# Kernel tuning notes

Measured on AMD Instinct MI355X. Metric: run time of the kernel, lower is better.

The kernel has to match this reference:

```python
import jax, jax.numpy as jnp
import numpy as np

NUM_HEADS = 8


def _nearest_idx(x, x_grid):
    # x: [b,n,dx]; x_grid: [b,H,W,dx] regular grid -> flat nearest cell index [b,n]
    b = x.shape[0]
    H, W = x_grid.shape[1], x_grid.shape[2]
    gf = x_grid.reshape(b, H * W, -1)
    lo = gf[:, :1]   # min corner [b,1,dx]
    hi = gf[:, -1:]  # max corner [b,1,dx]
    dims = jnp.asarray([H, W], dtype=x.dtype)
    t = (x - lo) / (hi - lo) * (dims - 1.0)
    idx = jnp.clip(jnp.round(t), 0.0, dims - 1.0).astype(jnp.int32)  # [b,n,2]
    return idx[..., 0] * W + idx[..., 1]


def _cumcount(idx):
    # per-batch cumulative count of each value, in order of appearance
    b, n = idx.shape
    order = jnp.argsort(idx, axis=1, stable=True)
    s = jnp.take_along_axis(idx, order, axis=1)
    ar = jnp.arange(n)
    new_run = jnp.concatenate([jnp.ones((b, 1), bool), s[:, 1:] != s[:, :-1]], axis=1)
    run_start = jax.lax.cummax(jnp.where(new_run, ar, 0), axis=1)
    cc_sorted = (ar - run_start).astype(jnp.int32)
    return jnp.zeros((b, n), jnp.int32).at[jnp.arange(b)[:, None], order].set(cc_sorted)


def _mhca(q_in, kv, mask, Wq, Wk, Wv, Wo):
    # q_in: [B,1,e]; kv: [B,K,e]; mask: [B,K] (True = attend)
    B, K, e = kv.shape
    dh = e // NUM_HEADS
    q = (q_in @ Wq).reshape(B, 1, NUM_HEADS, dh)
    k = (kv @ Wk).reshape(B, K, NUM_HEADS, dh)
    v = (kv @ Wv).reshape(B, K, NUM_HEADS, dh)
    scores = jnp.einsum('bqhd,bkhd->bhqk', q, k) / jnp.sqrt(jnp.asarray(dh, q.dtype))
    scores = jnp.where(mask[:, None, None, :], scores, jnp.finfo(scores.dtype).min)
    attn = jax.nn.softmax(scores, axis=-1)
    out = jnp.einsum('bhqk,bkhd->bqhd', attn, v).reshape(B, 1, e)
    return out @ Wo


def setup_inputs() -> dict:
    key = jax.random.key(0)
    ks = jax.random.split(key, 8)
    b, n, e, H, W = 8, 8192, 128, 64, 64
    x = jax.random.uniform(ks[0], (b, n, 2), jnp.float32)
    z = jax.random.normal(ks[1], (b, n, e), jnp.float32)
    g0 = jnp.linspace(0.0, 1.0, H)
    g1 = jnp.linspace(0.0, 1.0, W)
    mg = jnp.stack(jnp.meshgrid(g0, g1, indexing='ij'), axis=-1)  # [H,W,2]
    x_grid = jnp.broadcast_to(mg, (b, H, W, 2)).astype(jnp.float32)
    z_grid = jax.random.normal(ks[2], (b, H, W, e), jnp.float32)
    latent = jax.random.normal(ks[3], (e,), jnp.float32)
    scale = 1.0 / np.sqrt(e).astype(np.float32)
    Wq = jax.random.normal(ks[4], (e, e), jnp.float32) * scale
    Wk = jax.random.normal(ks[5], (e, e), jnp.float32) * scale
    Wv = jax.random.normal(ks[6], (e, e), jnp.float32) * scale
    Wo = jax.random.normal(ks[7], (e, e), jnp.float32) * scale
    return {"x": x, "z": z, "x_grid": x_grid, "z_grid": z_grid, "latent": latent,
            "Wq": Wq, "Wk": Wk, "Wv": Wv, "Wo": Wo, "max_patch": 20}


def reference(x, z, x_grid, z_grid, latent, Wq, Wk, Wv, Wo, max_patch):
    b, n, e = z.shape
    H, W = x_grid.shape[1], x_grid.shape[2]
    S = H * W
    nearest = _nearest_idx(x, x_grid)                    # [b,n]
    cc = _cumcount(nearest)                              # [b,n]
    bidx = jnp.broadcast_to(jnp.arange(b)[:, None], (b, n))
    valid = cc < max_patch
    slot = jnp.where(valid, cc, 0)
    # ragged scatter: pack each point's z into its grid cell's padded sequence
    joint = jnp.zeros((b, S, max_patch, e), z.dtype)
    joint = joint.at[bidx, nearest, slot].add(z * valid[..., None].astype(z.dtype))
    zg_flat = z_grid.reshape(b, S, e)
    joint = jnp.concatenate([joint, zg_flat[:, :, None, :]], axis=2)  # [b,S,P+1,e]
    counts = jnp.zeros((b, S), jnp.int32).at[bidx, nearest].add(1)
    mask = jnp.arange(max_patch + 1)[None, None, :] < jnp.minimum(counts, max_patch)[..., None]
    mask = mask.at[..., -1].set(True)  # grid token always attended
    joint = joint.reshape(b * S, max_patch + 1, e)
    mask = mask.reshape(b * S, max_patch + 1)
    q = jnp.broadcast_to(latent, (b * S, 1, e))          # z0_grid queries
    zg = _mhca(q, joint, mask, Wq, Wk, Wv, Wo)           # [b*S,1,e]
    zg = zg.reshape(b, H, W, e)
    return x_grid, zg
```

## Files before the change

### kernel.cpp

```cpp
#include <hip/hip_runtime.h>
#include <cstdint>
#include <cstddef>

#define S_CELLS 4096
#define NB      8
#define NPTS    8192
#define E       128
#define MAXP    20
#define NHEADS  8
#define NPT_ROWS 65536
#define NGR_ROWS 32768

#define WS_COUNTS 0
#define WS_SLOTS  131072
#define WS_WT1    2752512
#define WS_WT2    2793472
#define WS_SC     2828288
#define WS_V      5974016

typedef __attribute__((ext_vector_type(8))) short bf16x8;
typedef __attribute__((ext_vector_type(4))) float f32x4;

__device__ __forceinline__ unsigned short f2bf_bits(float f) {
    unsigned u = __float_as_uint(f);
    unsigned rounded = u + 0x7FFFu + ((u >> 16) & 1u);
    return (unsigned short)(rounded >> 16);
}
__device__ __forceinline__ float bf2f(unsigned short u) {
    return __uint_as_float(((unsigned)u) << 16);
}

__global__ void __launch_bounds__(256)
k_prep(const float* __restrict__ x,
       const float* __restrict__ x_grid,
       const float* __restrict__ latent,
       const float* __restrict__ Wq,
       const float* __restrict__ Wk,
       const float* __restrict__ Wv,
       const float* __restrict__ Wo,
       int* __restrict__ counts,
       int* __restrict__ slots,
       unsigned short* __restrict__ WT1,
       unsigned short* __restrict__ WT2,
       float* __restrict__ out_xgrid) {
    const int t   = threadIdx.x;
    const int blk = blockIdx.x;

    if (blk < 256) {
        int i = blk * 256 + t;
        out_xgrid[i] = x_grid[i];
        int b = i >> 13;
        float x0 = x[(size_t)i * 2 + 0];
        float x1 = x[(size_t)i * 2 + 1];
        int i0 = (int)rintf(x0 * 63.0f);
        int i1 = (int)rintf(x1 * 63.0f);
        i0 = min(max(i0, 0), 63);
        i1 = min(max(i1, 0), 63);
        int cell = b * S_CELLS + i0 * 64 + i1;
        int slot = atomicAdd(&counts[cell], 1);
        if (slot < MAXP) slots[(size_t)cell * MAXP + slot] = i & (NPTS - 1);
        return;
    }

    if (blk == 256) {
        __shared__ float lat[E];
        __shared__ float qv[E];
        const int j = t & 127;
        if (t < E) lat[t] = latent[t];
        __syncthreads();
        float acc = 0.0f;
        for (int k2 = 0; k2 < E; ++k2) acc += lat[k2] * Wq[k2 * E + j];
        qv[j] = acc;
        __syncthreads();
        const int hb = (t >> 7) * 4;
        for (int h = hb; h < hb + 4; ++h) {
            float a = 0.0f;
            #pragma unroll
            for (int d = 0; d < 16; ++d) a += Wk[j * E + h * 16 + d] * qv[h * 16 + d];
            WT1[(size_t)(128 + h) * 136 + j] = f2bf_bits(a * 0.25f);
        }
        for (int idx = t; idx < 8 * 136; idx += 256) {
            int rr = idx / 136, cc = idx - rr * 136;
            WT1[(size_t)(136 + rr) * 136 + cc] = 0;
        }
        return;
    }

    {
        const float* W = (blk < 261) ? Wv : Wo;
        unsigned short* WT = (blk < 261) ? WT1 : WT2;
        const int n0 = ((blk - 257) & 3) * 32;
        __shared__ float lbuf[128][33];
        #pragma unroll
        for (int it = 0; it < 16; ++it) {
            int k  = (t >> 5) + it * 8;
            int nl = t & 31;
            lbuf[k][nl] = W[(size_t)k * E + n0 + nl];
        }
        __syncthreads();
        for (int idx = t; idx < 32 * 136; idx += 256) {
            int nl = idx / 136, k = idx - nl * 136;
            float v = (k < 128) ? lbuf[k][nl] : 0.0f;
            WT[(size_t)(n0 + nl) * 136 + k] = f2bf_bits(v);
        }
    }
}

__device__ __forceinline__ bf16x8 load_afrag_f32(const float* __restrict__ X,
                                                 int row, int kq, int q) {
    const float4* xr = (const float4*)(X + (size_t)row * E);
    float4 lo = xr[kq * 8 + q * 2];
    float4 hi = xr[kq * 8 + q * 2 + 1];
    bf16x8 f;
    f[0] = (short)f2bf_bits(lo.x);
    f[1] = (short)f2bf_bits(lo.y);
    f[2] = (short)f2bf_bits(lo.z);
    f[3] = (short)f2bf_bits(lo.w);
    f[4] = (short)f2bf_bits(hi.x);
    f[5] = (short)f2bf_bits(hi.y);
    f[6] = (short)f2bf_bits(hi.z);
    f[7] = (short)f2bf_bits(hi.w);
    return f;
}

__global__ void __launch_bounds__(256)
k_gemm1(const float* __restrict__ Xz,
        const float* __restrict__ Xg,
        const unsigned short* __restrict__ WT1g,
        unsigned short* __restrict__ V,
        float* __restrict__ SC) {
    __shared__ unsigned short W_t[20480];

    const int t = threadIdx.x;
    {
        const float4* src = (const float4*)WT1g;
        float4* dst = (float4*)W_t;
        #pragma unroll
        for (int it = 0; it < 10; ++it) dst[t + it * 256] = src[t + it * 256];
    }
    __syncthreads();

    const int lane = t & 63;
    const int wv   = t >> 6;
    const int cn   = lane & 15;
    const int q    = lane >> 4;

    const int grow0 = blockIdx.x * 128;
    const float* Xsrc;
    int srow;
    if (blockIdx.x < 512) { Xsrc = Xz; srow = grow0; }
    else                  { Xsrc = Xg; srow = grow0 - NPT_ROWS; }

    f32x4 acc[2][9];
    #pragma unroll
    for (int mt = 0; mt < 2; ++mt)
        #pragma unroll
        for (int nt = 0; nt < 9; ++nt)
            acc[mt][nt] = f32x4{0.0f, 0.0f, 0.0f, 0.0f};

    #pragma unroll
    for (int kq = 0; kq < 4; ++kq) {
        bf16x8 a[2];
        #pragma unroll
        for (int mt = 0; mt < 2; ++mt)
            a[mt] = load_afrag_f32(Xsrc, srow + wv * 32 + mt * 16 + cn, kq, q);
        #pragma unroll
        for (int nt = 0; nt < 9; ++nt) {
            const bf16x8 b = *(const bf16x8*)&W_t[(size_t)(nt * 16 + cn) * 136 + kq * 32 + q * 8];
            #pragma unroll
            for (int mt = 0; mt < 2; ++mt)
                acc[mt][nt] = __builtin_amdgcn_mfma_f32_16x16x32_bf16(
                    a[mt], b, acc[mt][nt], 0, 0, 0);
        }
    }

    #pragma unroll
    for (int mt = 0; mt < 2; ++mt) {
        const int rb = grow0 + wv * 32 + mt * 16 + q * 4;
        #pragma unroll
        for (int nt = 0; nt < 8; ++nt)
            #pragma unroll
            for (int r = 0; r < 4; ++r)
                V[(size_t)(rb + r) * E + nt * 16 + cn] = f2bf_bits(acc[mt][nt][r]);
        if (cn < 8) {
            #pragma unroll
            for (int r = 0; r < 4; ++r)
                SC[(size_t)(rb + r) * NHEADS + cn] = acc[mt][8][r];
        }
    }
}

__global__ void __launch_bounds__(256)
k_attn_proj(const int* __restrict__ counts,
            const int* __restrict__ slots,
            const float* __restrict__ SC,
            const unsigned short* __restrict__ Vg,
            const unsigned short* __restrict__ WT2g,
            float* __restrict__ zg) {
    __shared__ unsigned short W_t[17408];
    __shared__ unsigned short X_s[16][136];

    const int t = threadIdx.x;
    {
        const float4* src = (const float4*)WT2g;
        float4* dst = (float4*)W_t;
        #pragma unroll
        for (int it = 0; it < 8; ++it) dst[t + it * 256] = src[t + it * 256];
        if (t < 128) dst[t + 2048] = src[t + 2048];
    }

    const int lane = t & 63;
    const int wv   = t >> 6;
    const int cb   = blockIdx.x * 16;
    const int cw   = cb + wv * 4;
    const int b    = blockIdx.x >> 8;
    const int base = b * NPTS;
    const int h    = lane >> 3;

    int cnt_l = (lane < 16) ? counts[cb + lane] : 0;

    int m4[4], sl[4];
    #pragma unroll
    for (int ci = 0; ci < 4; ++ci) {
        m4[ci] = min(__shfl(cnt_l, wv * 4 + ci, 64), MAXP);
        sl[ci] = (lane < MAXP) ? slots[(size_t)(cw + ci) * MAXP + lane] : 0;
    }

    float mm[4], ss[4], o0[4], o1[4];
    #pragma unroll
    for (int ci = 0; ci < 4; ++ci) {
        size_t r0 = (size_t)(NPT_ROWS + cw + ci);
        mm[ci] = SC[r0 * NHEADS + h];
        unsigned v0 = *(const unsigned*)(Vg + r0 * E + 2 * lane);
        o0[ci] = bf2f((unsigned short)v0);
        o1[ci] = bf2f((unsigned short)(v0 >> 16));
        ss[ci] = 1.0f;
    }

    #pragma unroll
    for (int ci = 0; ci < 4; ++ci) {
        const int m = m4[ci];
        for (int t0 = 0; t0 < m; t0 += 4) {
            float av[4], p0[4], p1[4];
            #pragma unroll
            for (int j = 0; j < 4; ++j) {
                int pt = __shfl(sl[ci], t0 + j, 64);
                bool val = (t0 + j) < m;
                pt = val ? pt : 0;
                size_t r = (size_t)(base + pt);
                float sa = SC[r * NHEADS + h];
                av[j] = val ? sa : -1e30f;
                unsigned vv = *(const unsigned*)(Vg + r * E + 2 * lane);
                p0[j] = bf2f((unsigned short)vv);
                p1[j] = bf2f((unsigned short)(vv >> 16));
            }
            #pragma unroll
            for (int j = 0; j < 4; ++j) {
                float nm = fmaxf(mm[ci], av[j]);
                float e  = __expf(av[j] - nm);
                float al = __expf(mm[ci] - nm);
                ss[ci] = ss[ci] * al + e;
                o0[ci] = o0[ci] * al + e * p0[j];
                o1[ci] = o1[ci] * al + e * p1[j];
                mm[ci] = nm;
            }
        }
        float inv = 1.0f / ss[ci];
        unsigned packed = (unsigned)f2bf_bits(o0[ci] * inv)
                        | ((unsigned)f2bf_bits(o1[ci] * inv) << 16);
        *(unsigned*)&X_s[wv * 4 + ci][2 * lane] = packed;
    }
    __syncthreads();

    const int cn  = lane & 15;
    const int q   = lane >> 4;
    const int nt0 = wv * 2;
    f32x4 acc[2];
    acc[0] = f32x4{0.0f, 0.0f, 0.0f, 0.0f};
    acc[1] = f32x4{0.0f, 0.0f, 0.0f, 0.0f};

    #pragma unroll
    for (int kq = 0; kq < 4; ++kq) {
        bf16x8 a = *(const bf16x8*)&X_s[cn][kq * 32 + q * 8];
        #pragma unroll
        for (int j = 0; j < 2; ++j) {
            const bf16x8 bb = *(const bf16x8*)&W_t[(size_t)((nt0 + j) * 16 + cn) * 136 + kq * 32 + q * 8];
            acc[j] = __builtin_amdgcn_mfma_f32_16x16x32_bf16(a, bb, acc[j], 0, 0, 0);
        }
    }

    const int rb = blockIdx.x * 16 + q * 4;
    #pragma unroll
    for (int j = 0; j < 2; ++j)
        #pragma unroll
        for (int r = 0; r < 4; ++r)
            zg[(size_t)(rb + r) * E + (nt0 + j) * 16 + cn] = acc[j][r];
}

extern "C" void kernel_launch(void* const* d_in, const int* in_sizes, int n_in,
                              void* d_out, int out_size, void* d_ws, size_t ws_size,
                              hipStream_t stream) {
    const float* x      = (const float*)d_in[0];
    const float* z      = (const float*)d_in[1];
    const float* x_grid = (const float*)d_in[2];
    const float* z_grid = (const float*)d_in[3];
    const float* latent = (const float*)d_in[4];
    const float* Wq     = (const float*)d_in[5];
    const float* Wk     = (const float*)d_in[6];
    const float* Wv     = (const float*)d_in[7];
    const float* Wo     = (const float*)d_in[8];

    char* ws = (char*)d_ws;
    int*            counts = (int*)(ws + WS_COUNTS);
    int*            slots  = (int*)(ws + WS_SLOTS);
    unsigned short* WT1    = (unsigned short*)(ws + WS_WT1);
    unsigned short* WT2    = (unsigned short*)(ws + WS_WT2);
    float*          SC     = (float*)(ws + WS_SC);
    unsigned short* V      = (unsigned short*)(ws + WS_V);

    float* out_xgrid = (float*)d_out;
    float* zg        = (float*)d_out + NB * NPTS;

    (void)hipMemsetAsync(counts, 0, NB * S_CELLS * sizeof(int), stream);

    k_prep<<<265, 256, 0, stream>>>(x, x_grid, latent, Wq, Wk, Wv, Wo,
                                    counts, slots, WT1, WT2, out_xgrid);

    k_gemm1<<<768, 256, 0, stream>>>(z, z_grid, WT1, V, SC);

    k_attn_proj<<<2048, 256, 0, stream>>>(counts, slots, SC, V, WT2, zg);
}
```

Measured before the change: 139.9 us.

## Fuse binning into GEMM kernel, drop memset, one wave per cell in attention

Zeroing of the cell counts moves into the small prep kernel, which replaces the memset. The point-binning blocks move into the main GEMM launch so they run alongside the projection work. The attention kernel now uses 1024-thread blocks with one wave per cell, and keeps the Wo fragments in registers loaded straight from global memory instead of staging them in LDS. BF16 packing switches to cheaper round-half-away conversion. This cuts launches, LDS staging and serial per-wave cell loops, at the cost of slightly different rounding and larger blocks that may reduce occupancy flexibility.

```diff
diff --git a/kernel.cpp b/kernel.cpp
--- a/kernel.cpp
+++ b/kernel.cpp
@@ -26,43 +26,37 @@
     unsigned rounded = u + 0x7FFFu + ((u >> 16) & 1u);
     return (unsigned short)(rounded >> 16);
 }
+__device__ __forceinline__ unsigned short f2bf_rta(float f) {
+    return (unsigned short)((__float_as_uint(f) + 0x8000u) >> 16);
+}
+__device__ __forceinline__ unsigned pack_bf2(float a, float b) {
+    unsigned ua = __float_as_uint(a) + 0x8000u;
+    unsigned ub = __float_as_uint(b) + 0x8000u;
+    return (ua >> 16) | (ub & 0xFFFF0000u);
+}
 __device__ __forceinline__ float bf2f(unsigned short u) {
     return __uint_as_float(((unsigned)u) << 16);
 }
 
 __global__ void __launch_bounds__(256)
-k_prep(const float* __restrict__ x,
-       const float* __restrict__ x_grid,
-       const float* __restrict__ latent,
+k_prep(const float* __restrict__ latent,
        const float* __restrict__ Wq,
        const float* __restrict__ Wk,
        const float* __restrict__ Wv,
        const float* __restrict__ Wo,
        int* __restrict__ counts,
-       int* __restrict__ slots,
        unsigned short* __restrict__ WT1,
-       unsigned short* __restrict__ WT2,
-       float* __restrict__ out_xgrid) {
+       unsigned short* __restrict__ WT2) {
     const int t   = threadIdx.x;
     const int blk = blockIdx.x;
 
-    if (blk < 256) {
-        int i = blk * 256 + t;
-        out_xgrid[i] = x_grid[i];
-        int b = i >> 13;
-        float x0 = x[(size_t)i * 2 + 0];
-        float x1 = x[(size_t)i * 2 + 1];
-        int i0 = (int)rintf(x0 * 63.0f);
-        int i1 = (int)rintf(x1 * 63.0f);
-        i0 = min(max(i0, 0), 63);
-        i1 = min(max(i1, 0), 63);
-        int cell = b * S_CELLS + i0 * 64 + i1;
-        int slot = atomicAdd(&counts[cell], 1);
-        if (slot < MAXP) slots[(size_t)cell * MAXP + slot] = i & (NPTS - 1);
-        return;
-    }
-
-    if (blk == 256) {
+    {
+        int4* c4 = (int4*)counts;
+        for (int idx = blk * 256 + t; idx < 8192; idx += 9 * 256)
+            c4[idx] = int4{0, 0, 0, 0};
+    }
+
+    if (blk == 0) {
         __shared__ float lat[E];
         __shared__ float qv[E];
         const int j = t & 127;
@@ -86,23 +80,21 @@
         return;
     }
 
-    {
-        const float* W = (blk < 261) ? Wv : Wo;
-        unsigned short* WT = (blk < 261) ? WT1 : WT2;
-        const int n0 = ((blk - 257) & 3) * 32;
-        __shared__ float lbuf[128][33];
-        #pragma unroll
-        for (int it = 0; it < 16; ++it) {
-            int k  = (t >> 5) + it * 8;
-            int nl = t & 31;
-            lbuf[k][nl] = W[(size_t)k * E + n0 + nl];
-        }
-        __syncthreads();
-        for (int idx = t; idx < 32 * 136; idx += 256) {
-            int nl = idx / 136, k = idx - nl * 136;
-            float v = (k < 128) ? lbuf[k][nl] : 0.0f;
-            WT[(size_t)(n0 + nl) * 136 + k] = f2bf_bits(v);
-        }
+    const float* W = (blk < 5) ? Wv : Wo;
+    unsigned short* WT = (blk < 5) ? WT1 : WT2;
+    const int n0 = ((blk - 1) & 3) * 32;
+    __shared__ float lbuf[128][33];
+    #pragma unroll
+    for (int it = 0; it < 16; ++it) {
+        int k  = (t >> 5) + it * 8;
+        int nl = t & 31;
+        lbuf[k][nl] = W[(size_t)k * E + n0 + nl];
+    }
+    __syncthreads();
+    for (int idx = t; idx < 32 * 136; idx += 256) {
+        int nl = idx / 136, k = idx - nl * 136;
+        float v = (k < 128) ? lbuf[k][nl] : 0.0f;
+        WT[(size_t)(n0 + nl) * 136 + k] = f2bf_bits(v);
     }
 }
 
@@ -111,27 +103,47 @@
     const float4* xr = (const float4*)(X + (size_t)row * E);
     float4 lo = xr[kq * 8 + q * 2];
     float4 hi = xr[kq * 8 + q * 2 + 1];
-    bf16x8 f;
-    f[0] = (short)f2bf_bits(lo.x);
-    f[1] = (short)f2bf_bits(lo.y);
-    f[2] = (short)f2bf_bits(lo.z);
-    f[3] = (short)f2bf_bits(lo.w);
-    f[4] = (short)f2bf_bits(hi.x);
-    f[5] = (short)f2bf_bits(hi.y);
-    f[6] = (short)f2bf_bits(hi.z);
-    f[7] = (short)f2bf_bits(hi.w);
-    return f;
+    unsigned u[4];
+    u[0] = pack_bf2(lo.x, lo.y);
+    u[1] = pack_bf2(lo.z, lo.w);
+    u[2] = pack_bf2(hi.x, hi.y);
+    u[3] = pack_bf2(hi.z, hi.w);
+    union { unsigned u4[4]; bf16x8 v; } cv;
+    cv.u4[0] = u[0]; cv.u4[1] = u[1]; cv.u4[2] = u[2]; cv.u4[3] = u[3];
+    return cv.v;
 }
 
 __global__ void __launch_bounds__(256)
-k_gemm1(const float* __restrict__ Xz,
-        const float* __restrict__ Xg,
-        const unsigned short* __restrict__ WT1g,
-        unsigned short* __restrict__ V,
-        float* __restrict__ SC) {
+k_main(const float* __restrict__ x,
+       const float* __restrict__ x_grid,
+       const float* __restrict__ Xz,
+       const float* __restrict__ Xg,
+       const unsigned short* __restrict__ WT1g,
+       int* __restrict__ counts,
+       int* __restrict__ slots,
+       unsigned short* __restrict__ V,
+       float* __restrict__ SC,
+       float* __restrict__ out_xgrid) {
     __shared__ unsigned short W_t[20480];
 
     const int t = threadIdx.x;
+
+    if (blockIdx.x >= 768) {
+        int i = (blockIdx.x - 768) * 256 + t;
+        out_xgrid[i] = x_grid[i];
+        int b = i >> 13;
+        float x0 = x[(size_t)i * 2 + 0];
+        float x1 = x[(size_t)i * 2 + 1];
+        int i0 = (int)rintf(x0 * 63.0f);
+        int i1 = (int)rintf(x1 * 63.0f);
+        i0 = min(max(i0, 0), 63);
+        i1 = min(max(i1, 0), 63);
+        int cell = b * S_CELLS + i0 * 64 + i1;
+        int slot = atomicAdd(&counts[cell], 1);
+        if (slot < MAXP) slots[(size_t)cell * MAXP + slot] = i & (NPTS - 1);
+        return;
+    }
+
     {
         const float4* src = (const float4*)WT1g;
         float4* dst = (float4*)W_t;
@@ -181,7 +193,7 @@
         for (int nt = 0; nt < 8; ++nt)
             #pragma unroll
             for (int r = 0; r < 4; ++r)
-                V[(size_t)(rb + r) * E + nt * 16 + cn] = f2bf_bits(acc[mt][nt][r]);
+                V[(size_t)(rb + r) * E + nt * 16 + cn] = f2bf_rta(acc[mt][nt][r]);
         if (cn < 8) {
             #pragma unroll
             for (int r = 0; r < 4; ++r)
@@ -190,111 +202,83 @@
     }
 }
 
-__global__ void __launch_bounds__(256)
+__global__ void __launch_bounds__(1024)
 k_attn_proj(const int* __restrict__ counts,
             const int* __restrict__ slots,
             const float* __restrict__ SC,
             const unsigned short* __restrict__ Vg,
             const unsigned short* __restrict__ WT2g,
             float* __restrict__ zg) {
-    __shared__ unsigned short W_t[17408];
-    __shared__ unsigned short X_s[16][136];
-
-    const int t = threadIdx.x;
-    {
-        const float4* src = (const float4*)WT2g;
-        float4* dst = (float4*)W_t;
-        #pragma unroll
-        for (int it = 0; it < 8; ++it) dst[t + it * 256] = src[t + it * 256];
-        if (t < 128) dst[t + 2048] = src[t + 2048];
-    }
-
+    __shared__ __align__(16) unsigned short X_s[16][136];
+
+    const int t    = threadIdx.x;
     const int lane = t & 63;
     const int wv   = t >> 6;
     const int cb   = blockIdx.x * 16;
-    const int cw   = cb + wv * 4;
-    const int b    = blockIdx.x >> 8;
+    const int b    = cb >> 12;
     const int base = b * NPTS;
-    const int h    = lane >> 3;
-
-    int cnt_l = (lane < 16) ? counts[cb + lane] : 0;
-
-    int m4[4], sl[4];
-    #pragma unroll
-    for (int ci = 0; ci < 4; ++ci) {
-        m4[ci] = min(__shfl(cnt_l, wv * 4 + ci, 64), MAXP);
-        sl[ci] = (lane < MAXP) ? slots[(size_t)(cw + ci) * MAXP + lane] : 0;
-    }
-
-    float mm[4], ss[4], o0[4], o1[4];
-    #pragma unroll
-    for (int ci = 0; ci < 4; ++ci) {
-        size_t r0 = (size_t)(NPT_ROWS + cw + ci);
-        mm[ci] = SC[r0 * NHEADS + h];
-        unsigned v0 = *(const unsigned*)(Vg + r0 * E + 2 * lane);
-        o0[ci] = bf2f((unsigned short)v0);
-        o1[ci] = bf2f((unsigned short)(v0 >> 16));
-        ss[ci] = 1.0f;
-    }
-
-    #pragma unroll
-    for (int ci = 0; ci < 4; ++ci) {
-        const int m = m4[ci];
-        for (int t0 = 0; t0 < m; t0 += 4) {
-            float av[4], p0[4], p1[4];
-            #pragma unroll
-            for (int j = 0; j < 4; ++j) {
-                int pt = __shfl(sl[ci], t0 + j, 64);
-                bool val = (t0 + j) < m;
-                pt = val ? pt : 0;
-                size_t r = (size_t)(base + pt);
-                float sa = SC[r * NHEADS + h];
-                av[j] = val ? sa : -1e30f;
-                unsigned vv = *(const unsigned*)(Vg + r * E + 2 * lane);
-                p0[j] = bf2f((unsigned short)vv);
-                p1[j] = bf2f((unsigned short)(vv >> 16));
-            }
-            #pragma unroll
-            for (int j = 0; j < 4; ++j) {
-                float nm = fmaxf(mm[ci], av[j]);
-                float e  = __expf(av[j] - nm);
-                float al = __expf(mm[ci] - nm);
-                ss[ci] = ss[ci] * al + e;
-                o0[ci] = o0[ci] * al + e * p0[j];
-                o1[ci] = o1[ci] * al + e * p1[j];
-                mm[ci] = nm;
-            }
-        }
-        float inv = 1.0f / ss[ci];
-        unsigned packed = (unsigned)f2bf_bits(o0[ci] * inv)
-                        | ((unsigned)f2bf_bits(o1[ci] * inv) << 16);
-        *(unsigned*)&X_s[wv * 4 + ci][2 * lane] = packed;
-    }
+    const int cn   = lane & 15;
+    const int q    = lane >> 4;
+
+    bf16x8 bfr[4];
+    if (wv < 8) {
+        #pragma unroll
+        for (int kq = 0; kq < 4; ++kq)
+            bfr[kq] = *(const bf16x8*)&WT2g[(size_t)(wv * 16 + cn) * 136 + kq * 32 + q * 8];
+    }
+
+    const int cell = cb + wv;
+    const int m    = min(counts[cell], MAXP);
+    int sl = (lane < MAXP) ? slots[(size_t)cell * MAXP + lane] : 0;
+    const int h = lane >> 3;
+
+    size_t r0 = (size_t)(NPT_ROWS + cell);
+    float mm = SC[r0 * NHEADS + h];
+    float ss = 1.0f;
+    unsigned v0 = *(const unsigned*)(Vg + r0 * E + 2 * lane);
+    float o0 = bf2f((unsigned short)v0);
+    float o1 = bf2f((unsigned short)(v0 >> 16));
+
+    for (int t0 = 0; t0 < m; t0 += 4) {
+        float av[4], p0[4], p1[4];
+        #pragma unroll
+        for (int j = 0; j < 4; ++j) {
+            int pt = __shfl(sl, t0 + j, 64);
+            bool val = (t0 + j) < m;
+            pt = val ? pt : 0;
+            size_t r = (size_t)(base + pt);
+            float sa = SC[r * NHEADS + h];
+            av[j] = val ? sa : -1e30f;
+            unsigned vv = *(const unsigned*)(Vg + r * E + 2 * lane);
+            p0[j] = bf2f((unsigned short)vv);
+            p1[j] = bf2f((unsigned short)(vv >> 16));
+        }
+        #pragma unroll
+        for (int j = 0; j < 4; ++j) {
+            float nm = fmaxf(mm, av[j]);
+            float e  = __expf(av[j] - nm);
+            float al = __expf(mm - nm);
+            ss = ss * al + e;
+            o0 = o0 * al + e * p0[j];
+            o1 = o1 * al + e * p1[j];
+            mm = nm;
+        }
+    }
+    float inv = 1.0f / ss;
+    *(unsigned*)&X_s[wv][2 * lane] = pack_bf2(o0 * inv, o1 * inv);
     __syncthreads();
 
-    const int cn  = lane & 15;
-    const int q   = lane >> 4;
-    const int nt0 = wv * 2;
-    f32x4 acc[2];
-    acc[0] = f32x4{0.0f, 0.0f, 0.0f, 0.0f};
-    acc[1] = f32x4{0.0f, 0.0f, 0.0f, 0.0f};
-
-    #pragma unroll
-    for (int kq = 0; kq < 4; ++kq) {
-        bf16x8 a = *(const bf16x8*)&X_s[cn][kq * 32 + q * 8];
-        #pragma unroll
-        for (int j = 0; j < 2; ++j) {
-            const bf16x8 bb = *(const bf16x8*)&W_t[(size_t)((nt0 + j) * 16 + cn) * 136 + kq * 32 + q * 8];
-            acc[j] = __builtin_amdgcn_mfma_f32_16x16x32_bf16(a, bb, acc[j], 0, 0, 0);
-        }
-    }
-
-    const int rb = blockIdx.x * 16 + q * 4;
-    #pragma unroll
-    for (int j = 0; j < 2; ++j)
+    if (wv < 8) {
+        f32x4 acc = f32x4{0.0f, 0.0f, 0.0f, 0.0f};
+        #pragma unroll
+        for (int kq = 0; kq < 4; ++kq) {
+            bf16x8 a = *(const bf16x8*)&X_s[cn][kq * 32 + q * 8];
+            acc = __builtin_amdgcn_mfma_f32_16x16x32_bf16(a, bfr[kq], acc, 0, 0, 0);
+        }
         #pragma unroll
         for (int r = 0; r < 4; ++r)
-            zg[(size_t)(rb + r) * E + (nt0 + j) * 16 + cn] = acc[j][r];
+            zg[(size_t)(cb + q * 4 + r) * E + wv * 16 + cn] = acc[r];
+    }
 }
 
 extern "C" void kernel_launch(void* const* d_in, const int* in_sizes, int n_in,
@@ -321,12 +305,10 @@
     float* out_xgrid = (float*)d_out;
     float* zg        = (float*)d_out + NB * NPTS;
 
-    (void)hipMemsetAsync(counts, 0, NB * S_CELLS * sizeof(int), stream);
-
-    k_prep<<<265, 256, 0, stream>>>(x, x_grid, latent, Wq, Wk, Wv, Wo,
-                                    counts, slots, WT1, WT2, out_xgrid);
-
-    k_gemm1<<<768, 256, 0, stream>>>(z, z_grid, WT1, V, SC);
-
-    k_attn_proj<<<2048, 256, 0, stream>>>(counts, slots, SC, V, WT2, zg);
-}
+    k_prep<<<9, 256, 0, stream>>>(latent, Wq, Wk, Wv, Wo, counts, WT1, WT2);
+
+    k_main<<<1024, 256, 0, stream>>>(x, x_grid, z, z_grid, WT1,
+                                     counts, slots, V, SC, out_xgrid);
+
+    k_attn_proj<<<2048, 1024, 0, stream>>>(counts, slots, SC, V, WT2, zg);
+}
```

After: 137.1 us. 2.0% less time.
